# Optimization experiments

Hardware: AMD Instinct MI355X
Metric: run time of the kernel (lower is better)

Reference implementation:

```python
import jax, jax.numpy as jnp
import numpy as np

N_NODES = 100000
N_EDGES = 1600000
N_GRAPHS = 64
BN_EPS = 1e-5


def setup_inputs() -> dict:
    key = jax.random.key(0)
    ks = jax.random.split(key, 16)
    inp = {
        'x': jax.random.normal(ks[0], (N_NODES, 768), dtype=jnp.float32),
        'edge_index': jax.random.randint(ks[1], (2, N_EDGES), 0, N_NODES, dtype=jnp.int32),
        'batch': jnp.sort(jax.random.randint(ks[2], (N_NODES,), 0, N_GRAPHS, dtype=jnp.int32)),
        'W_in': jax.random.normal(ks[3], (768, 256), dtype=jnp.float32) * 0.02,
        'b_in': jax.random.normal(ks[4], (256,), dtype=jnp.float32) * 0.02,
        'W_g': jax.random.normal(ks[5], (3, 256, 256), dtype=jnp.float32) * 0.05,
        'b_g': jax.random.normal(ks[6], (3, 256), dtype=jnp.float32) * 0.02,
        'bn_gamma': jax.random.uniform(ks[7], (3, 256), dtype=jnp.float32) + 0.5,
        'bn_beta': jax.random.normal(ks[8], (3, 256), dtype=jnp.float32) * 0.02,
        'bn_mean': jax.random.normal(ks[9], (3, 256), dtype=jnp.float32) * 0.02,
        'bn_var': jax.random.uniform(ks[10], (3, 256), dtype=jnp.float32) + 0.5,
        'W1': jax.random.normal(ks[11], (256, 128), dtype=jnp.float32) * 0.06,
        'b1': jax.random.normal(ks[12], (128,), dtype=jnp.float32) * 0.02,
        'W2': jax.random.normal(ks[13], (128, 128), dtype=jnp.float32) * 0.08,
        'b2': jax.random.normal(ks[14], (128,), dtype=jnp.float32) * 0.02,
    }
    return inp


def reference(x, edge_index, batch, W_in, b_in, W_g, b_g, bn_gamma, bn_beta,
              bn_mean, bn_var, W1, b1, W2, b2):
    N = x.shape[0]
    # Add self loops (PyG GCNConv default)
    loop = jnp.arange(N, dtype=edge_index.dtype)
    src = jnp.concatenate([edge_index[0], loop])  # [E+N]
    dst = jnp.concatenate([edge_index[1], loop])
    # Symmetric GCN normalization: deg over dst after self loops
    deg = jax.ops.segment_sum(jnp.ones_like(src, dtype=x.dtype), dst, num_segments=N)
    dinv = jnp.where(deg > 0, jax.lax.rsqrt(deg), 0.0)
    norm = (dinv[src] * dinv[dst])[:, None]  # [E+N, 1]

    # input projection + relu
    h = jax.nn.relu(x @ W_in + b_in)  # [N, 256]

    for i in range(W_g.shape[0]):
        m = h @ W_g[i]                                   # [N, 256]
        agg = jax.ops.segment_sum(m[src] * norm, dst, num_segments=N) + b_g[i]
        # BatchNorm (eval mode, running stats)
        agg = (agg - bn_mean[i]) * (bn_gamma[i] * jax.lax.rsqrt(bn_var[i] + BN_EPS)) + bn_beta[i]
        h = jax.nn.relu(agg)  # dropout is identity in eval

    # global mean pool per graph
    sums = jax.ops.segment_sum(h, batch, num_segments=N_GRAPHS)       # [G, 256]
    cnts = jax.ops.segment_sum(jnp.ones((N,), x.dtype), batch, num_segments=N_GRAPHS)
    g = sums / jnp.maximum(cnts, 1.0)[:, None]

    # output MLP
    out = jax.nn.relu(g @ W1 + b1) @ W2 + b2  # [G, 128]
    return out
```

## Files before the change

kernel.cpp:

```cpp
#include <hip/hip_runtime.h>
#include <hip/hip_fp16.h>

#define HIDDEN 256

using bfrag = __attribute__((ext_vector_type(8))) short;
using hfrag = __attribute__((ext_vector_type(8))) _Float16;
using facc16 = __attribute__((ext_vector_type(16))) float;

#define BARRIER_LGKM()                                   \
  do {                                                   \
    asm volatile("s_waitcnt lgkmcnt(0)" ::: "memory");   \
    __builtin_amdgcn_s_barrier();                        \
  } while (0)

__device__ inline short bf16_rne(float x) {
  unsigned u = __builtin_bit_cast(unsigned, x);
  unsigned r = u + 0x7FFFu + ((u >> 16) & 1u);
  return (short)(r >> 16);
}
__device__ inline float bf16_to_f(short h) {
  unsigned u = ((unsigned)(unsigned short)h) << 16;
  return __builtin_bit_cast(float, u);
}
__device__ inline float h2f(unsigned short h) {
  return __half2float(__builtin_bit_cast(__half, h));
}
__device__ inline unsigned short f2h_bits(float v) {
  return __builtin_bit_cast(unsigned short, __float2half(v));
}
__device__ inline void cvt8(const float4& a, const float4& b, bfrag& hi, bfrag& lo) {
  float av[8] = {a.x, a.y, a.z, a.w, b.x, b.y, b.z, b.w};
#pragma unroll
  for (int i = 0; i < 8; ++i) {
    unsigned u = __builtin_bit_cast(unsigned, av[i]);
    hi[i] = (short)(u >> 16);
    float r = av[i] - __builtin_bit_cast(float, u & 0xFFFF0000u);
    lo[i] = (short)(__builtin_bit_cast(unsigned, r) >> 16);
  }
}

__global__ __launch_bounds__(256) void k_scan_a(const int* __restrict__ deg,
                                                int* __restrict__ bsum, int N) {
  const int t = threadIdx.x, lane = t & 63, w = t >> 6;
  const int idx = blockIdx.x * 256 + t;
  int x = (idx < N) ? deg[idx] : 0;
#pragma unroll
  for (int off = 32; off >= 1; off >>= 1) x += __shfl_xor(x, off);
  __shared__ int ws[4];
  if (lane == 0) ws[w] = x;
  __syncthreads();
  if (t == 0) bsum[blockIdx.x] = ws[0] + ws[1] + ws[2] + ws[3];
}

__global__ __launch_bounds__(512) void k_scan_b(const int* __restrict__ bsum,
                                                int* __restrict__ boff, int nb) {
  const int t = threadIdx.x, lane = t & 63, w = t >> 6;
  int orig = (t < nb) ? bsum[t] : 0;
  int x = orig;
#pragma unroll
  for (int off = 1; off < 64; off <<= 1) {
    int y = __shfl_up(x, off);
    if (lane >= off) x += y;
  }
  __shared__ int wsum[8];
  if (lane == 63) wsum[w] = x;
  __syncthreads();
  if (w == 0 && lane < 8) {
    int s = wsum[lane];
#pragma unroll
    for (int off = 1; off < 8; off <<= 1) {
      int y = __shfl_up(s, off);
      if (lane >= off) s += y;
    }
    wsum[lane] = s;
  }
  __syncthreads();
  int inc = x + (w > 0 ? wsum[w - 1] : 0);
  if (t < nb) boff[t] = inc - orig;
}

__global__ __launch_bounds__(256) void k_scan_c(const int* __restrict__ deg,
                                                const int* __restrict__ boff,
                                                int* __restrict__ row_ptr,
                                                float* __restrict__ dinv, int N) {
  const int t = threadIdx.x, lane = t & 63, w = t >> 6;
  const int idx = blockIdx.x * 256 + t;
  int d = (idx < N) ? deg[idx] : 0;
  int x = d;
#pragma unroll
  for (int off = 1; off < 64; off <<= 1) {
    int y = __shfl_up(x, off);
    if (lane >= off) x += y;
  }
  __shared__ int ws[4];
  if (lane == 63) ws[w] = x;
  __syncthreads();
  int add = boff[blockIdx.x];
#pragma unroll
  for (int j = 0; j < 4; ++j)
    if (j < w) add += ws[j];
  if (idx < N) {
    row_ptr[idx + 1] = x + add;
    dinv[idx] = 1.0f / sqrtf((float)d + 1.0f);
  }
  if (idx == 0) row_ptr[0] = 0;
}

__global__ __launch_bounds__(256) void k_prep_w(const float* __restrict__ W_in,
                                                const float* __restrict__ W_g,
                                                short* __restrict__ Wt) {
  const int e = blockIdx.x * blockDim.x + threadIdx.x;
  if (e >= 196608 + 3 * 65536) return;
  float v;
  int k, n;
  size_t base;
  bool isproj;
  if (e < 196608) {
    k = e >> 8;
    n = e & 255;
    v = W_in[e];
    base = 0;
    isproj = true;
  } else {
    int r = e - 196608;
    int lyr = r >> 16;
    k = (r >> 8) & 255;
    n = r & 255;
    v = W_g[r];
    base = 393216 + (size_t)lyr * 131072;
    isproj = false;
  }
  size_t pos = base + (size_t)(k >> 5) * 16384 + (size_t)n * 32 + (k & 31);
  if (isproj) {
    short hi = bf16_rne(v);
    short lo = bf16_rne(v - bf16_to_f(hi));
    Wt[pos] = hi;
    Wt[pos + 8192] = lo;
  } else {
    __half hh = __float2half(v);
    float r = v - __half2float(hh);
    Wt[pos] = (short)__builtin_bit_cast(unsigned short, hh);
    Wt[pos + 8192] = (short)__builtin_bit_cast(unsigned short, __float2half(r));
  }
}

__device__ __forceinline__ void proj_body(int bx, const float* __restrict__ A,
                                          const short* __restrict__ Wt,
                                          const float* __restrict__ bias,
                                          unsigned short* __restrict__ Ch,
                                          int M, int K) {
  __shared__ short As[2][64][66];
  const int t = threadIdx.x;
  const int w = t >> 6, l = t & 63;
  const int g2 = l >> 5, l31 = l & 31;
  const int row0 = bx * 64;
  const int colbase = w * 64;
  const int arow = t >> 2, ak = (t & 3) << 3;

  facc16 acc[2][2];
#pragma unroll
  for (int i = 0; i < 2; ++i)
#pragma unroll
    for (int j = 0; j < 2; ++j) acc[i][j] = (facc16)(0.0f);

  const int nsteps = K >> 5;
  const int ga = row0 + arow;
  const bool aval = ga < M;
  const float* aptr = A + (size_t)ga * K + ak;

  float4 f0 = make_float4(0.f, 0.f, 0.f, 0.f), f1 = f0;
  if (aval) {
    f0 = *(const float4*)aptr;
    f1 = *(const float4*)(aptr + 4);
  }
  {
    bfrag hi, lo;
    cvt8(f0, f1, hi, lo);
    *(bfrag*)&As[0][arow][ak] = hi;
    *(bfrag*)&As[0][arow][32 + ak] = lo;
  }
  if (nsteps > 1 && aval) {
    f0 = *(const float4*)(aptr + 32);
    f1 = *(const float4*)(aptr + 36);
  }

  int cur = 0;
  for (int s = 0; s < nsteps; ++s) {
    BARRIER_LGKM();
    bfrag bh[2][2], bl[2][2];
#pragma unroll
    for (int nt = 0; nt < 2; ++nt)
#pragma unroll
      for (int kh = 0; kh < 2; ++kh) {
        const short* wbp = Wt + ((size_t)s << 14) +
                           (size_t)(colbase + nt * 32 + l31) * 32 + kh * 16 + g2 * 8;
        bh[nt][kh] = *(const bfrag*)wbp;
        bl[nt][kh] = *(const bfrag*)(wbp + 8192);
      }
#pragma unroll
    for (int kh = 0; kh < 2; ++kh) {
      bfrag ah[2], al[2];
#pragma unroll
      for (int mt = 0; mt < 2; ++mt) {
        ah[mt] = *(const bfrag*)&As[cur][mt * 32 + l31][kh * 16 + g2 * 8];
        al[mt] = *(const bfrag*)&As[cur][mt * 32 + l31][32 + kh * 16 + g2 * 8];
      }
#pragma unroll
      for (int mt = 0; mt < 2; ++mt)
#pragma unroll
        for (int nt = 0; nt < 2; ++nt)
          acc[mt][nt] = __builtin_amdgcn_mfma_f32_32x32x16_bf16(
              ah[mt], bh[nt][kh], acc[mt][nt], 0, 0, 0);
#pragma unroll
      for (int mt = 0; mt < 2; ++mt)
#pragma unroll
        for (int nt = 0; nt < 2; ++nt)
          acc[mt][nt] = __builtin_amdgcn_mfma_f32_32x32x16_bf16(
              ah[mt], bl[nt][kh], acc[mt][nt], 0, 0, 0);
#pragma unroll
      for (int mt = 0; mt < 2; ++mt)
#pragma unroll
        for (int nt = 0; nt < 2; ++nt)
          acc[mt][nt] = __builtin_amdgcn_mfma_f32_32x32x16_bf16(
              al[mt], bh[nt][kh], acc[mt][nt], 0, 0, 0);
    }
    if (s + 1 < nsteps) {
      bfrag hi, lo;
      cvt8(f0, f1, hi, lo);
      *(bfrag*)&As[cur ^ 1][arow][ak] = hi;
      *(bfrag*)&As[cur ^ 1][arow][32 + ak] = lo;
      if (s + 2 < nsteps && aval) {
        const float* ap = aptr + (size_t)(s + 2) * 32;
        f0 = *(const float4*)ap;
        f1 = *(const float4*)(ap + 4);
      }
    }
    cur ^= 1;
  }
#pragma unroll
  for (int nt = 0; nt < 2; ++nt) {
    const int col = colbase + nt * 32 + l31;
    const float b = bias[col];
#pragma unroll
    for (int mt = 0; mt < 2; ++mt)
#pragma unroll
      for (int r = 0; r < 16; ++r) {
        int row = row0 + mt * 32 + (r & 3) + 8 * (r >> 2) + 4 * g2;
        if (row < M)
          Ch[(size_t)row * HIDDEN + col] = f2h_bits(fmaxf(acc[mt][nt][r] + b, 0.f));
      }
  }
}

#define LG_LOAD(S, AA, BH, BL)                                          \
  {                                                                     \
    AA[0][0] = *(const hfrag*)(ap0 + (S) * 32);                         \
    AA[0][1] = *(const hfrag*)(ap0 + (S) * 32 + 16);                    \
    AA[1][0] = *(const hfrag*)(ap1 + (S) * 32);                         \
    AA[1][1] = *(const hfrag*)(ap1 + (S) * 32 + 16);                    \
    const short* wp = wb + ((size_t)(S) << 14);                         \
    BH[0][0] = *(const hfrag*)(wp);                                     \
    BH[0][1] = *(const hfrag*)(wp + 16);                                \
    BH[1][0] = *(const hfrag*)(wp + 1024);                              \
    BH[1][1] = *(const hfrag*)(wp + 1024 + 16);                         \
    BL[0][0] = *(const hfrag*)(wp + 8192);                              \
    BL[0][1] = *(const hfrag*)(wp + 8192 + 16);                         \
    BL[1][0] = *(const hfrag*)(wp + 8192 + 1024);                       \
    BL[1][1] = *(const hfrag*)(wp + 8192 + 1024 + 16);                  \
  }

#define LG_COMPUTE(AA, BH, BL)                                          \
  _Pragma("unroll") for (int kh = 0; kh < 2; ++kh) {                    \
    _Pragma("unroll") for (int mt = 0; mt < 2; ++mt)                    \
        _Pragma("unroll") for (int nt = 0; nt < 2; ++nt) acc[mt][nt] =  \
        __builtin_amdgcn_mfma_f32_32x32x16_f16(AA[mt][kh], BH[nt][kh],  \
                                               acc[mt][nt], 0, 0, 0);   \
    _Pragma("unroll") for (int mt = 0; mt < 2; ++mt)                    \
        _Pragma("unroll") for (int nt = 0; nt < 2; ++nt) acc[mt][nt] =  \
        __builtin_amdgcn_mfma_f32_32x32x16_f16(AA[mt][kh], BL[nt][kh],  \
                                               acc[mt][nt], 0, 0, 0);   \
  }

__device__ __forceinline__ void layer_gemm_body(
    int bx, const unsigned short* __restrict__ A, const short* __restrict__ Wt,
    const float* __restrict__ dinv, unsigned short* __restrict__ Cm, int M) {
  const int t = threadIdx.x;
  const int w = t >> 6, l = t & 63;
  const int g2 = l >> 5, l31 = l & 31;
  const int row0 = bx * 64;
  const int colbase = w * 64;

  facc16 acc[2][2];
#pragma unroll
  for (int i = 0; i < 2; ++i)
#pragma unroll
    for (int j = 0; j < 2; ++j) acc[i][j] = (facc16)(0.0f);

  int r0 = row0 + l31, r1 = row0 + 32 + l31;
  if (r0 >= M) r0 = M - 1;
  if (r1 >= M) r1 = M - 1;
  const unsigned short* ap0 = A + (size_t)r0 * HIDDEN + g2 * 8;
  const unsigned short* ap1 = A + (size_t)r1 * HIDDEN + g2 * 8;
  const short* wb = Wt + (size_t)(colbase + l31) * 32 + g2 * 8;

  hfrag aA[2][2], bhA[2][2], blA[2][2];
  hfrag aB[2][2], bhB[2][2], blB[2][2];

  LG_LOAD(0, aA, bhA, blA);
#pragma unroll
  for (int s = 0; s < 8; s += 2) {
    if (s + 1 < 8) LG_LOAD(s + 1, aB, bhB, blB);
    LG_COMPUTE(aA, bhA, blA);
    if (s + 2 < 8) LG_LOAD(s + 2, aA, bhA, blA);
    LG_COMPUTE(aB, bhB, blB);
  }
#pragma unroll
  for (int mt = 0; mt < 2; ++mt)
#pragma unroll
    for (int r = 0; r < 16; ++r) {
      int row = row0 + mt * 32 + (r & 3) + 8 * (r >> 2) + 4 * g2;
      if (row >= M) continue;
      const float sc = dinv[row];
#pragma unroll
      for (int nt = 0; nt < 2; ++nt)
        Cm[(size_t)row * HIDDEN + colbase + nt * 32 + l31] =
            f2h_bits(acc[mt][nt][r] * sc);
    }
}

__global__ __launch_bounds__(256, 3) void k_mega1(
    const float* __restrict__ x, const short* __restrict__ Wt,
    const float* __restrict__ b_in, unsigned short* __restrict__ h0, int M,
    int K, const int* __restrict__ dst, int* __restrict__ deg, int E,
    int ngemm, int nhist) {
  if ((int)blockIdx.x < ngemm) {
    proj_body(blockIdx.x, x, Wt, b_in, h0, M, K);
  } else {
    const int b = blockIdx.x - ngemm;
    for (int e = b * 256 + threadIdx.x; e < E; e += nhist * 256)
      atomicAdd(&deg[dst[e]], 1);
  }
}

__global__ __launch_bounds__(256, 2) void k_mega2(
    const unsigned short* __restrict__ h0, const short* __restrict__ WtL,
    const float* __restrict__ dinv, unsigned short* __restrict__ h1, int M,
    const int* __restrict__ src, const int* __restrict__ dst,
    const int* __restrict__ row_ptr, int* __restrict__ fill,
    int* __restrict__ csr, int E, int ngemm, int nfill) {
  if ((int)blockIdx.x < ngemm) {
    layer_gemm_body(blockIdx.x, h0, WtL, dinv, h1, M);
  } else {
    const int b = blockIdx.x - ngemm;
    for (int e = b * 256 + threadIdx.x; e < E; e += nfill * 256) {
      int d = dst[e];
      int pos = atomicAdd(&fill[d], 1);
      csr[row_ptr[d] + pos] = src[e];
    }
  }
}

__global__ __launch_bounds__(256, 2) void k_gemm_layer(
    const unsigned short* __restrict__ h, const short* __restrict__ WtL,
    const float* __restrict__ dinv, unsigned short* __restrict__ m, int M) {
  layer_gemm_body(blockIdx.x, h, WtL, dinv, m, M);
}

__global__ __launch_bounds__(256) void k_aggregate(
    const unsigned short* __restrict__ mp, const int* __restrict__ row_ptr,
    const int* __restrict__ csr, const float* __restrict__ dinv,
    const float* __restrict__ bg, const float* __restrict__ gamma,
    const float* __restrict__ beta, const float* __restrict__ mean,
    const float* __restrict__ var, unsigned short* __restrict__ hout, int N) {
  const int wave = threadIdx.x >> 6, l = threadIdx.x & 63;
  const int v = blockIdx.x * 4 + wave;
  if (v >= N) return;
  const int co = l << 2;
  ushort4 rs = *(const ushort4*)(mp + (size_t)v * HIDDEN + co);
  float4 acc;
  acc.x = h2f(rs.x); acc.y = h2f(rs.y); acc.z = h2f(rs.z); acc.w = h2f(rs.w);
  const int s = row_ptr[v], e = row_ptr[v + 1];
  int i = s;
  for (; i + 8 <= e; i += 8) {
    ushort4 r0 = *(const ushort4*)(mp + (size_t)csr[i + 0] * HIDDEN + co);
    ushort4 r1 = *(const ushort4*)(mp + (size_t)csr[i + 1] * HIDDEN + co);
    ushort4 r2 = *(const ushort4*)(mp + (size_t)csr[i + 2] * HIDDEN + co);
    ushort4 r3 = *(const ushort4*)(mp + (size_t)csr[i + 3] * HIDDEN + co);
    ushort4 r4 = *(const ushort4*)(mp + (size_t)csr[i + 4] * HIDDEN + co);
    ushort4 r5 = *(const ushort4*)(mp + (size_t)csr[i + 5] * HIDDEN + co);
    ushort4 r6 = *(const ushort4*)(mp + (size_t)csr[i + 6] * HIDDEN + co);
    ushort4 r7 = *(const ushort4*)(mp + (size_t)csr[i + 7] * HIDDEN + co);
    acc.x += h2f(r0.x) + h2f(r1.x) + h2f(r2.x) + h2f(r3.x) +
             h2f(r4.x) + h2f(r5.x) + h2f(r6.x) + h2f(r7.x);
    acc.y += h2f(r0.y) + h2f(r1.y) + h2f(r2.y) + h2f(r3.y) +
             h2f(r4.y) + h2f(r5.y) + h2f(r6.y) + h2f(r7.y);
    acc.z += h2f(r0.z) + h2f(r1.z) + h2f(r2.z) + h2f(r3.z) +
             h2f(r4.z) + h2f(r5.z) + h2f(r6.z) + h2f(r7.z);
    acc.w += h2f(r0.w) + h2f(r1.w) + h2f(r2.w) + h2f(r3.w) +
             h2f(r4.w) + h2f(r5.w) + h2f(r6.w) + h2f(r7.w);
  }
  for (; i < e; ++i) {
    ushort4 r0 = *(const ushort4*)(mp + (size_t)csr[i] * HIDDEN + co);
    acc.x += h2f(r0.x);
    acc.y += h2f(r0.y);
    acc.z += h2f(r0.z);
    acc.w += h2f(r0.w);
  }
  const float dv = dinv[v];
  float4 bg4 = *(const float4*)&bg[co];
  float4 g4 = *(const float4*)&gamma[co];
  float4 be4 = *(const float4*)&beta[co];
  float4 mn4 = *(const float4*)&mean[co];
  float4 vr4 = *(const float4*)&var[co];
  ushort4 o;
  o.x = f2h_bits(fmaxf((acc.x * dv + bg4.x - mn4.x) * (g4.x / sqrtf(vr4.x + 1e-5f)) + be4.x, 0.f));
  o.y = f2h_bits(fmaxf((acc.y * dv + bg4.y - mn4.y) * (g4.y / sqrtf(vr4.y + 1e-5f)) + be4.y, 0.f));
  o.z = f2h_bits(fmaxf((acc.z * dv + bg4.z - mn4.z) * (g4.z / sqrtf(vr4.z + 1e-5f)) + be4.z, 0.f));
  o.w = f2h_bits(fmaxf((acc.w * dv + bg4.w - mn4.w) * (g4.w / sqrtf(vr4.w + 1e-5f)) + be4.w, 0.f));
  *(ushort4*)&hout[(size_t)v * HIDDEN + co] = o;
}

__global__ __launch_bounds__(64) void k_count(const int* __restrict__ batch,
                                              float* __restrict__ cnt, int N,
                                              int G) {
  const int g = threadIdx.x;
  if (g >= G) return;
  int lo = 0, hi = N;
  while (lo < hi) {
    int mid = (lo + hi) >> 1;
    if (batch[mid] < g) lo = mid + 1; else hi = mid;
  }
  int lo2 = lo, hi2 = N;
  while (lo2 < hi2) {
    int mid = (lo2 + hi2) >> 1;
    if (batch[mid] < g + 1) lo2 = mid + 1; else hi2 = mid;
  }
  cnt[g] = (float)(lo2 - lo);
}

__global__ __launch_bounds__(256) void k_pool(const unsigned short* __restrict__ h,
                                              const int* __restrict__ batch,
                                              float* __restrict__ sums, int N) {
  const int t = threadIdx.x;
  const int start = blockIdx.x * 256;
  if (start >= N) return;
  const int end = min(start + 256, N);
  float acc = 0.f;
  int cur = batch[start];
  for (int n = start; n < end; ++n) {
    int g = batch[n];
    if (g != cur) {
      atomicAdd(&sums[cur * HIDDEN + t], acc);
      acc = 0.f;
      cur = g;
    }
    acc += h2f(h[(size_t)n * HIDDEN + t]);
  }
  atomicAdd(&sums[cur * HIDDEN + t], acc);
}

__global__ __launch_bounds__(128) void k_head(const float* __restrict__ sums,
                                              const float* __restrict__ cnt,
                                              const float* __restrict__ W1,
                                              const float* __restrict__ b1,
                                              const float* __restrict__ W2,
                                              const float* __restrict__ b2,
                                              float* __restrict__ out) {
  __shared__ float gr[256];
  __shared__ float t1[128];
  const int b = blockIdx.x, t = threadIdx.x;
  const float inv = 1.0f / fmaxf(cnt[b], 1.0f);
  gr[t] = sums[b * HIDDEN + t] * inv;
  gr[t + 128] = sums[b * HIDDEN + t + 128] * inv;
  __syncthreads();
  float a = b1[t];
  for (int k = 0; k < 256; ++k) a += gr[k] * W1[k * 128 + t];
  t1[t] = fmaxf(a, 0.f);
  __syncthreads();
  float o = b2[t];
  for (int k = 0; k < 128; ++k) o += t1[k] * W2[k * 128 + t];
  out[b * 128 + t] = o;
}

extern "C" void kernel_launch(void* const* d_in, const int* in_sizes, int n_in,
                              void* d_out, int out_size, void* d_ws,
                              size_t ws_size, hipStream_t stream) {
  (void)n_in;
  (void)ws_size;
  const float* x = (const float*)d_in[0];
  const int* ei = (const int*)d_in[1];
  const int* batch = (const int*)d_in[2];
  const float* W_in = (const float*)d_in[3];
  const float* b_in = (const float*)d_in[4];
  const float* W_g = (const float*)d_in[5];
  const float* b_g = (const float*)d_in[6];
  const float* bn_gamma = (const float*)d_in[7];
  const float* bn_beta = (const float*)d_in[8];
  const float* bn_mean = (const float*)d_in[9];
  const float* bn_var = (const float*)d_in[10];
  const float* W1 = (const float*)d_in[11];
  const float* b1 = (const float*)d_in[12];
  const float* W2 = (const float*)d_in[13];
  const float* b2 = (const float*)d_in[14];

  const int KIN = 768;
  const int N = in_sizes[0] / KIN;
  const int E = in_sizes[1] / 2;
  const int G = out_size / 128;

  const int* src = ei;
  const int* dst = ei + E;

  char* ws = (char*)d_ws;
  size_t off = 0;
  auto take = [&](size_t bytes) -> void* {
    void* p = ws + off;
    off += (bytes + 255) & ~(size_t)255;
    return p;
  };
  unsigned short* h0 = (unsigned short*)take((size_t)N * HIDDEN * 2);
  unsigned short* h1 = (unsigned short*)take((size_t)N * HIDDEN * 2);
  float* dinv = (float*)take((size_t)N * 4);
  int* deg = (int*)take((size_t)N * 4);
  int* fill = (int*)take((size_t)N * 4);
  int* row_ptr = (int*)take((size_t)(N + 1) * 4);
  int* csr = (int*)take((size_t)E * 4);
  float* sums = (float*)take((size_t)G * HIDDEN * 4);
  float* cnt = (float*)take((size_t)G * 4);
  short* Wt = (short*)take((size_t)(393216 + 3 * 131072) * 2);
  const int nb = (N + 255) / 256;
  int* bsum = (int*)take((size_t)nb * 4);
  int* boff = (int*)take((size_t)nb * 4);

  hipMemsetAsync(deg, 0, (size_t)N * 4, stream);
  hipMemsetAsync(fill, 0, (size_t)N * 4, stream);
  hipMemsetAsync(sums, 0, (size_t)G * HIDDEN * 4, stream);

  const int gx = (N + 63) / 64;
  const int NH = 256;
  const int NF = 256;

  k_prep_w<<<(196608 + 3 * 65536 + 255) / 256, 256, 0, stream>>>(W_in, W_g, Wt);
  k_mega1<<<gx + NH, 256, 0, stream>>>(x, Wt, b_in, h0, N, KIN, dst, deg, E,
                                       gx, NH);
  k_scan_a<<<nb, 256, 0, stream>>>(deg, bsum, N);
  k_scan_b<<<1, 512, 0, stream>>>(bsum, boff, nb);
  k_scan_c<<<nb, 256, 0, stream>>>(deg, boff, row_ptr, dinv, N);
  k_mega2<<<gx + NF, 256, 0, stream>>>(h0, Wt + 393216, dinv, h1, N, src, dst,
                                       row_ptr, fill, csr, E, gx, NF);
  k_aggregate<<<(N + 3) / 4, 256, 0, stream>>>(
      h1, row_ptr, csr, dinv, b_g, bn_gamma, bn_beta, bn_mean, bn_var, h0, N);
  for (int i = 1; i < 3; ++i) {
    k_gemm_layer<<<gx, 256, 0, stream>>>(h0, Wt + 393216 + (size_t)i * 131072,
                                         dinv, h1, N);
    k_aggregate<<<(N + 3) / 4, 256, 0, stream>>>(
        h1, row_ptr, csr, dinv, b_g + i * HIDDEN, bn_gamma + i * HIDDEN,
        bn_beta + i * HIDDEN, bn_mean + i * HIDDEN, bn_var + i * HIDDEN, h0, N);
  }
  k_count<<<1, 64, 0, stream>>>(batch, cnt, N, G);
  k_pool<<<(N + 255) / 256, 256, 0, stream>>>(h0, batch, sums, N);
  k_head<<<G, 128, 0, stream>>>(sums, cnt, W1, b1, W2, b2, (float*)d_out);
}
```

Before: 988.1 us.

## Fuse GCN aggregation with next layer's GEMM via LDS-resident tile

Adds a kernel that gathers neighbor messages for a 64-row tile, applies bias/BatchNorm/ReLU, stores the activated tile in shared memory, then multiplies it by the next layer's weights with fp16 MFMA and writes the dinv-scaled messages. This replaces the separate aggregate and layer-GEMM launches for layers 1 and 2, removing one fp16 activation write and read per layer. The gather phase now runs with 64-row blocks and an LDS footprint of about 33KB, which may lower occupancy and latency hiding for the irregular gather compared to the 4-node-per-block aggregate kernel.

```diff
diff --git a/kernel.cpp b/kernel.cpp
--- a/kernel.cpp
+++ b/kernel.cpp
@@ -231,7 +231,7 @@
       *(bfrag*)&As[cur ^ 1][arow][32 + ak] = lo;
       if (s + 2 < nsteps && aval) {
         const float* ap = aptr + (size_t)(s + 2) * 32;
-        f0 = *(const float4*)ap;
+        f0 = *(const float4*)(ap + 0);
         f1 = *(const float4*)(ap + 4);
       }
     }
@@ -328,6 +328,134 @@
     }
 }
 
+__global__ __launch_bounds__(256, 4) void k_agg_gemm(
+    const unsigned short* __restrict__ mp, const int* __restrict__ row_ptr,
+    const int* __restrict__ csr, const float* __restrict__ dinv,
+    const float* __restrict__ bg, const float* __restrict__ gamma,
+    const float* __restrict__ beta, const float* __restrict__ mean,
+    const float* __restrict__ var, const short* __restrict__ WtL,
+    unsigned short* __restrict__ mout, int N) {
+  __shared__ unsigned short hl[64][264];
+  const int t = threadIdx.x;
+  const int w = t >> 6, l = t & 63;
+  const int row0 = blockIdx.x * 64;
+  const int co = l << 2;
+
+  float4 g4 = *(const float4*)&gamma[co];
+  float4 vr4 = *(const float4*)&var[co];
+  float4 bg4 = *(const float4*)&bg[co];
+  float4 mn4 = *(const float4*)&mean[co];
+  float4 be4 = *(const float4*)&beta[co];
+  float4 sc4, sh4;
+  sc4.x = g4.x / sqrtf(vr4.x + 1e-5f);
+  sc4.y = g4.y / sqrtf(vr4.y + 1e-5f);
+  sc4.z = g4.z / sqrtf(vr4.z + 1e-5f);
+  sc4.w = g4.w / sqrtf(vr4.w + 1e-5f);
+  sh4.x = (bg4.x - mn4.x) * sc4.x + be4.x;
+  sh4.y = (bg4.y - mn4.y) * sc4.y + be4.y;
+  sh4.z = (bg4.z - mn4.z) * sc4.z + be4.z;
+  sh4.w = (bg4.w - mn4.w) * sc4.w + be4.w;
+
+  for (int i = 0; i < 16; ++i) {
+    const int v = row0 + w * 16 + i;
+    ushort4 o = make_ushort4(0, 0, 0, 0);
+    if (v < N) {
+      ushort4 rs = *(const ushort4*)(mp + (size_t)v * HIDDEN + co);
+      float4 acc;
+      acc.x = h2f(rs.x); acc.y = h2f(rs.y); acc.z = h2f(rs.z); acc.w = h2f(rs.w);
+      const int s = row_ptr[v], e = row_ptr[v + 1];
+      int j = s;
+      for (; j + 8 <= e; j += 8) {
+        ushort4 r0 = *(const ushort4*)(mp + (size_t)csr[j + 0] * HIDDEN + co);
+        ushort4 r1 = *(const ushort4*)(mp + (size_t)csr[j + 1] * HIDDEN + co);
+        ushort4 r2 = *(const ushort4*)(mp + (size_t)csr[j + 2] * HIDDEN + co);
+        ushort4 r3 = *(const ushort4*)(mp + (size_t)csr[j + 3] * HIDDEN + co);
+        ushort4 r4 = *(const ushort4*)(mp + (size_t)csr[j + 4] * HIDDEN + co);
+        ushort4 r5 = *(const ushort4*)(mp + (size_t)csr[j + 5] * HIDDEN + co);
+        ushort4 r6 = *(const ushort4*)(mp + (size_t)csr[j + 6] * HIDDEN + co);
+        ushort4 r7 = *(const ushort4*)(mp + (size_t)csr[j + 7] * HIDDEN + co);
+        acc.x += h2f(r0.x) + h2f(r1.x) + h2f(r2.x) + h2f(r3.x) +
+                 h2f(r4.x) + h2f(r5.x) + h2f(r6.x) + h2f(r7.x);
+        acc.y += h2f(r0.y) + h2f(r1.y) + h2f(r2.y) + h2f(r3.y) +
+                 h2f(r4.y) + h2f(r5.y) + h2f(r6.y) + h2f(r7.y);
+        acc.z += h2f(r0.z) + h2f(r1.z) + h2f(r2.z) + h2f(r3.z) +
+                 h2f(r4.z) + h2f(r5.z) + h2f(r6.z) + h2f(r7.z);
+        acc.w += h2f(r0.w) + h2f(r1.w) + h2f(r2.w) + h2f(r3.w) +
+                 h2f(r4.w) + h2f(r5.w) + h2f(r6.w) + h2f(r7.w);
+      }
+      for (; j < e; ++j) {
+        ushort4 r0 = *(const ushort4*)(mp + (size_t)csr[j] * HIDDEN + co);
+        acc.x += h2f(r0.x);
+        acc.y += h2f(r0.y);
+        acc.z += h2f(r0.z);
+        acc.w += h2f(r0.w);
+      }
+      const float dv = dinv[v];
+      o.x = f2h_bits(fmaxf(acc.x * dv * sc4.x + sh4.x, 0.f));
+      o.y = f2h_bits(fmaxf(acc.y * dv * sc4.y + sh4.y, 0.f));
+      o.z = f2h_bits(fmaxf(acc.z * dv * sc4.z + sh4.z, 0.f));
+      o.w = f2h_bits(fmaxf(acc.w * dv * sc4.w + sh4.w, 0.f));
+    }
+    *(ushort4*)&hl[w * 16 + i][co] = o;
+  }
+  __syncthreads();
+
+  const int g2 = l >> 5, l31 = l & 31;
+  const int colbase = w * 64;
+  facc16 acc[2][2];
+#pragma unroll
+  for (int i = 0; i < 2; ++i)
+#pragma unroll
+    for (int j = 0; j < 2; ++j) acc[i][j] = (facc16)(0.0f);
+
+  const short* wb = WtL + (size_t)(colbase + l31) * 32 + g2 * 8;
+#pragma unroll
+  for (int s = 0; s < 8; ++s) {
+    const short* wp = wb + ((size_t)s << 14);
+    hfrag bh[2][2], bl[2][2], ah[2][2];
+#pragma unroll
+    for (int nt = 0; nt < 2; ++nt)
+#pragma unroll
+      for (int kh = 0; kh < 2; ++kh) {
+        bh[nt][kh] = *(const hfrag*)(wp + nt * 1024 + kh * 16);
+        bl[nt][kh] = *(const hfrag*)(wp + 8192 + nt * 1024 + kh * 16);
+      }
+#pragma unroll
+    for (int mt = 0; mt < 2; ++mt)
+#pragma unroll
+      for (int kh = 0; kh < 2; ++kh)
+        ah[mt][kh] =
+            *(const hfrag*)&hl[mt * 32 + l31][s * 32 + kh * 16 + g2 * 8];
+#pragma unroll
+    for (int kh = 0; kh < 2; ++kh) {
+#pragma unroll
+      for (int mt = 0; mt < 2; ++mt)
+#pragma unroll
+        for (int nt = 0; nt < 2; ++nt)
+          acc[mt][nt] = __builtin_amdgcn_mfma_f32_32x32x16_f16(
+              ah[mt][kh], bh[nt][kh], acc[mt][nt], 0, 0, 0);
+#pragma unroll
+      for (int mt = 0; mt < 2; ++mt)
+#pragma unroll
+        for (int nt = 0; nt < 2; ++nt)
+          acc[mt][nt] = __builtin_amdgcn_mfma_f32_32x32x16_f16(
+              ah[mt][kh], bl[nt][kh], acc[mt][nt], 0, 0, 0);
+    }
+  }
+#pragma unroll
+  for (int mt = 0; mt < 2; ++mt)
+#pragma unroll
+    for (int r = 0; r < 16; ++r) {
+      int row = row0 + mt * 32 + (r & 3) + 8 * (r >> 2) + 4 * g2;
+      if (row >= N) continue;
+      const float sc = dinv[row];
+#pragma unroll
+      for (int nt = 0; nt < 2; ++nt)
+        mout[(size_t)row * HIDDEN + colbase + nt * 32 + l31] =
+            f2h_bits(acc[mt][nt][r] * sc);
+    }
+}
+
 __global__ __launch_bounds__(256, 3) void k_mega1(
     const float* __restrict__ x, const short* __restrict__ Wt,
     const float* __restrict__ b_in, unsigned short* __restrict__ h0, int M,
@@ -358,12 +486,6 @@
       csr[row_ptr[d] + pos] = src[e];
     }
   }
-}
-
-__global__ __launch_bounds__(256, 2) void k_gemm_layer(
-    const unsigned short* __restrict__ h, const short* __restrict__ WtL,
-    const float* __restrict__ dinv, unsigned short* __restrict__ m, int M) {
-  layer_gemm_body(blockIdx.x, h, WtL, dinv, m, M);
 }
 
 __global__ __launch_bounds__(256) void k_aggregate(
@@ -519,7 +641,8 @@
     return p;
   };
   unsigned short* h0 = (unsigned short*)take((size_t)N * HIDDEN * 2);
-  unsigned short* h1 = (unsigned short*)take((size_t)N * HIDDEN * 2);
+  unsigned short* m1 = (unsigned short*)take((size_t)N * HIDDEN * 2);
+  unsigned short* m2 = (unsigned short*)take((size_t)N * HIDDEN * 2);
   float* dinv = (float*)take((size_t)N * 4);
   int* deg = (int*)take((size_t)N * 4);
   int* fill = (int*)take((size_t)N * 4);
@@ -546,17 +669,18 @@
   k_scan_a<<<nb, 256, 0, stream>>>(deg, bsum, N);
   k_scan_b<<<1, 512, 0, stream>>>(bsum, boff, nb);
   k_scan_c<<<nb, 256, 0, stream>>>(deg, boff, row_ptr, dinv, N);
-  k_mega2<<<gx + NF, 256, 0, stream>>>(h0, Wt + 393216, dinv, h1, N, src, dst,
+  k_mega2<<<gx + NF, 256, 0, stream>>>(h0, Wt + 393216, dinv, m1, N, src, dst,
                                        row_ptr, fill, csr, E, gx, NF);
+  k_agg_gemm<<<gx, 256, 0, stream>>>(m1, row_ptr, csr, dinv, b_g, bn_gamma,
+                                     bn_beta, bn_mean, bn_var,
+                                     Wt + 393216 + 131072, m2, N);
+  k_agg_gemm<<<gx, 256, 0, stream>>>(
+      m1 == m2 ? m2 : m2, row_ptr, csr, dinv, b_g + HIDDEN, bn_gamma + HIDDEN,
+      bn_beta + HIDDEN, bn_mean + HIDDEN, bn_var + HIDDEN,
+      Wt + 393216 + 2 * 131072, m1, N);
   k_aggregate<<<(N + 3) / 4, 256, 0, stream>>>(
-      h1, row_ptr, csr, dinv, b_g, bn_gamma, bn_beta, bn_mean, bn_var, h0, N);
-  for (int i = 1; i < 3; ++i) {
-    k_gemm_layer<<<gx, 256, 0, stream>>>(h0, Wt + 393216 + (size_t)i * 131072,
-                                         dinv, h1, N);
-    k_aggregate<<<(N + 3) / 4, 256, 0, stream>>>(
-        h1, row_ptr, csr, dinv, b_g + i * HIDDEN, bn_gamma + i * HIDDEN,
-        bn_beta + i * HIDDEN, bn_mean + i * HIDDEN, bn_var + i * HIDDEN, h0, N);
-  }
+      m1, row_ptr, csr, dinv, b_g + 2 * HIDDEN, bn_gamma + 2 * HIDDEN,
+      bn_beta + 2 * HIDDEN, bn_mean + 2 * HIDDEN, bn_var + 2 * HIDDEN, h0, N);
   k_count<<<1, 64, 0, stream>>>(batch, cnt, N, G);
   k_pool<<<(N + 255) / 256, 256, 0, stream>>>(h0, batch, sums, N);
   k_head<<<G, 128, 0, stream>>>(sums, cnt, W1, b1, W2, b2, (float*)d_out);
```

New measurement: 1.004 ms. Within noise of the previous version (+1.6%).
